# Kernel optimization log

Hardware: AMD Instinct MI355X
Metric: run time of the kernel (lower is better)

## Reference

```python
import jax, jax.numpy as jnp
import numpy as np

N_U, N_I, D = 30000, 15000, 64
L = 2                 # propagation layers (self.l)
TEMP = 0.2
LAMBDA1, LAMBDA2 = 0.2, 1e-7
H, F = 4, 16          # GAT heads x per-head dim; H*F == D
NEG_SLOPE = 0.2
AVG_DEG = 16
B = 2048


def setup_inputs() -> dict:
    key = jax.random.key(0)
    ks = jax.random.split(key, 10)
    rng = np.random.default_rng(0)
    E_u_0 = jax.random.normal(ks[0], (N_U, D), jnp.float32) * 0.1
    E_i_0 = jax.random.normal(ks[1], (N_I, D), jnp.float32) * 0.1
    # sparse normalized bipartite adjacency (adj_norm) as an edge list
    nnz = N_U * AVG_DEG
    u_idx = np.repeat(np.arange(N_U), AVG_DEG)
    i_idx = rng.integers(0, N_I, nnz)
    deg_u = np.bincount(u_idx, minlength=N_U)
    deg_i = np.maximum(np.bincount(i_idx, minlength=N_I), 1)
    vals = (1.0 / np.sqrt(deg_u[u_idx] * deg_i[i_idx])).astype(np.float32)
    # GAT graph on n_u+n_i nodes: bipartite edges both directions + self-loops
    n = N_U + N_I
    src = np.concatenate([u_idx, i_idx + N_U, np.arange(n)]).astype(np.int32)
    dst = np.concatenate([i_idx + N_U, u_idx, np.arange(n)]).astype(np.int32)
    # GAT parameters (fresh each forward in original, so just random)
    W = jax.random.normal(ks[2], (D, H * F), jnp.float32) / np.sqrt(D)
    attn_l = jax.random.normal(ks[3], (H, F), jnp.float32) * 0.1
    attn_r = jax.random.normal(ks[4], (H, F), jnp.float32) * 0.1
    uids = jax.random.randint(ks[5], (B,), 0, N_U, jnp.int32)
    iids = jax.random.randint(ks[6], (B,), 0, N_I, jnp.int32)
    pos = jax.random.randint(ks[7], (B,), 0, N_I, jnp.int32)
    neg = jax.random.randint(ks[8], (B,), 0, N_I, jnp.int32)
    return dict(E_u_0=E_u_0, E_i_0=E_i_0, adj_vals=jnp.asarray(vals),
                W=W, attn_l=attn_l, attn_r=attn_r,
                u_idx=jnp.asarray(u_idx, jnp.int32), i_idx=jnp.asarray(i_idx, jnp.int32),
                src=jnp.asarray(src), dst=jnp.asarray(dst),
                uids=uids, iids=iids, pos=pos, neg=neg)


def gat_layer(h, src, dst, W, attn_l, attn_r, n_nodes):
    # GATConv: project, per-edge attention, neighborhood softmax, scatter-agg
    feat = (h @ W).reshape(-1, H, F)                      # [N,H,F]
    el = (feat * attn_l).sum(-1)                          # [N,H]
    er = (feat * attn_r).sum(-1)                          # [N,H]
    e = jax.nn.leaky_relu(el[src] + er[dst], NEG_SLOPE)   # [E,H]
    e_max = jax.ops.segment_max(e, dst, num_segments=n_nodes)
    a = jnp.exp(e - e_max[dst])
    denom = jax.ops.segment_sum(a, dst, num_segments=n_nodes)
    a = a / denom[dst]                                    # self-loops => denom>0
    out = jax.ops.segment_sum(a[:, :, None] * feat[src], dst, num_segments=n_nodes)
    return jax.nn.elu(out.reshape(-1, H * F))             # [N,D]


def _forward(E_u_0, E_i_0, adj_vals, W, attn_l, attn_r,
             u_idx, i_idx, src, dst, uids, iids, pos, neg):
    n = N_U + N_I
    Eu, Ei = E_u_0, E_i_0
    sum_Eu, sum_Ei = E_u_0, E_i_0
    sum_Gu, sum_Gi = E_u_0, E_i_0
    for _ in range(L):
        # LightGCN spmm propagation: Z_u = A @ E_i, Z_i = A.T @ E_u
        Zu = jax.ops.segment_sum(adj_vals[:, None] * Ei[i_idx], u_idx, num_segments=N_U)
        Zi = jax.ops.segment_sum(adj_vals[:, None] * Eu[u_idx], i_idx, num_segments=N_I)
        ls1 = gat_layer(jnp.concatenate([Eu, Ei], 0), src, dst, W, attn_l, attn_r, n)
        Gu, Gi = ls1[:N_U], ls1[N_U:]
        Eu, Ei = Zu + Eu, Zi + Ei
        sum_Eu = sum_Eu + Eu
        sum_Ei = sum_Ei + Ei
        sum_Gu = sum_Gu + Gu
        sum_Gi = sum_Gi + Gi
    log_eps = jnp.float32(np.log(1e-8))
    # InfoNCE: log(sum(exp(s)) + 1e-8) == logaddexp(logsumexp(s), log(1e-8))
    lse_u = jax.scipy.special.logsumexp(sum_Gu[uids] @ sum_Eu.T / TEMP, axis=1)
    lse_i = jax.scipy.special.logsumexp(sum_Gi[iids] @ sum_Ei.T / TEMP, axis=1)
    neg_score = jnp.logaddexp(lse_u, log_eps).mean() + jnp.logaddexp(lse_i, log_eps).mean()
    pos_score = ((sum_Gu[uids] * sum_Eu[uids]).sum(1) / TEMP).mean() \
              + ((sum_Gi[iids] * sum_Ei[iids]).sum(1) / TEMP).mean()
    loss_s = -pos_score + neg_score
    # BPR loss
    u_emb = sum_Eu[uids]
    diff = (u_emb * sum_Ei[pos]).sum(-1) - (u_emb * sum_Ei[neg]).sum(-1)
    loss_r = -jax.nn.log_sigmoid(diff).mean()
    # L2 reg over nn.Parameters (E_u_0, E_i_0 only)
    loss_reg = LAMBDA2 * ((E_u_0 ** 2).sum() + (E_i_0 ** 2).sum())
    loss = loss_r + LAMBDA1 * loss_s + loss_reg
    return loss, loss_r, LAMBDA1 * loss_s


def reference(E_u_0, E_i_0, adj_vals, W, attn_l, attn_r,
              u_idx, i_idx, src, dst, uids, iids, pos, neg):
    return _forward(E_u_0, E_i_0, adj_vals, W, attn_l, attn_r,
                    u_idx, i_idx, src, dst, uids, iids, pos, neg)
```

## Files before the change

kernel.cpp:

```cpp
#include <hip/hip_runtime.h>
#include <math.h>

#define N_U 30000
#define N_I 15000
#define N_TOT 45000
#define D 64
#define NNZ 480000
#define B 2048
#define INV_TEMP 5.0f
#define LOG_EPS -18.420680743952367f
#define NEG_SLOPE 0.2f
#define LAMBDA1 0.2f
#define LAMBDA2 1e-7f

#define NSP 128
#define RSP_U 235
#define RSP_I 118
#define PAD_U 30016
#define PAD_I 15040
#define SCALE_LOG2 7.2134752044448170f
#define LN2F 0.6931471805599453f

typedef __attribute__((ext_vector_type(8))) short short8;
typedef __attribute__((ext_vector_type(4))) float f32x4;

__device__ inline float wred(float v) {
#pragma unroll
  for (int o = 32; o > 0; o >>= 1) v += __shfl_down(v, o, 64);
  return v;
}

__device__ inline float leaky(float v) { return (v >= 0.f) ? v : NEG_SLOPE * v; }

__device__ inline void atomMaxF(float* a, float v) {
  if (v >= 0.f) atomicMax((int*)a, __float_as_int(v));
  else atomicMin((unsigned int*)a, __float_as_uint(v));
}

__device__ inline unsigned short f2bf(float x) {
  unsigned u = __float_as_uint(x);
  unsigned r = u + 0x7FFFu + ((u >> 16) & 1u);
  return (unsigned short)(r >> 16);
}
__device__ inline float bf2f(unsigned short h) {
  return __uint_as_float(((unsigned)h) << 16);
}

__global__ void k_init(const float* __restrict__ Eu0, const float* __restrict__ Ei0,
                       float* fU, float* fI, float* sEu, float* sEi,
                       float* sGu, float* sGi, int* deg, float* acc) {
  int t = blockIdx.x * 256 + threadIdx.x;
  if (t < 16) acc[t] = (t >= 8) ? -INFINITY : 0.f;
  if (t < N_I) deg[t] = 0;
  if (t < N_U * D) {
    int n = t >> 6, c = t & 63;
    float v = Eu0[t];
    fU[(size_t)n * 128 + c] = v;
    sEu[t] = v; sGu[t] = v;
  } else if (t < N_TOT * D) {
    int j = t - N_U * D;
    int n = j >> 6, c = j & 63;
    float v = Ei0[j];
    fI[(size_t)n * 128 + c] = v;
    sEi[j] = v; sGi[j] = v;
  }
}

__global__ void k_deg(const int* __restrict__ ii, int* deg) {
  int e = blockIdx.x * 256 + threadIdx.x;
  if (e < NNZ) atomicAdd(&deg[ii[e]], 1);
}

__global__ void k_scan(const int* __restrict__ deg, int* rowptr, int* cursor) {
  __shared__ int tsum[1024];
  const int CHUNK = 15;
  int tid = threadIdx.x;
  int base = tid * CHUNK;
  int s = 0;
#pragma unroll
  for (int k = 0; k < CHUNK; k++) {
    int idx = base + k;
    s += (idx < N_I) ? deg[idx] : 0;
  }
  tsum[tid] = s;
  __syncthreads();
  for (int o = 1; o < 1024; o <<= 1) {
    int x = (tid >= o) ? tsum[tid - o] : 0;
    __syncthreads();
    tsum[tid] += x;
    __syncthreads();
  }
  int excl = tsum[tid] - s;
#pragma unroll
  for (int k = 0; k < CHUNK; k++) {
    int idx = base + k;
    if (idx < N_I) {
      rowptr[idx] = excl;
      cursor[idx] = excl;
      excl += deg[idx];
    }
  }
  if (tid == 1023) rowptr[N_I] = tsum[1023];
}

__global__ void k_fill(const int* __restrict__ ii, const float* __restrict__ vals,
                       int* cursor, int* u_srt, float* v_srt) {
  int e = blockIdx.x * 256 + threadIdx.x;
  if (e < NNZ) {
    int pos = atomicAdd(&cursor[ii[e]], 1);
    u_srt[pos] = e >> 4;
    v_srt[pos] = vals[e];
  }
}

__global__ void k_feat(float* __restrict__ fU, float* __restrict__ fI,
                       const float* __restrict__ W, const float* __restrict__ al,
                       const float* __restrict__ ar,
                       float* __restrict__ el, float* __restrict__ er) {
  __shared__ float Ws[64 * 64];
  __shared__ float hs[16][64];
  int tid = threadIdx.x;
  for (int t = tid; t < 1024; t += 256) ((float4*)Ws)[t] = ((const float4*)W)[t];
  int g = tid >> 6, c = tid & 63;
  int n0 = blockIdx.x * 16 + g * 4;
  float* rows[4];
#pragma unroll
  for (int j = 0; j < 4; j++) {
    int node = n0 + j;
    rows[j] = nullptr;
    if (node < N_TOT) {
      rows[j] = (node < N_U) ? (fU + (size_t)node * 128) : (fI + (size_t)(node - N_U) * 128);
      hs[g * 4 + j][c] = rows[j][c];
    }
  }
  __syncthreads();
  float a0 = 0.f, a1 = 0.f, a2 = 0.f, a3 = 0.f;
#pragma unroll 8
  for (int k = 0; k < 64; ++k) {
    float w = Ws[k * 64 + c];
    a0 = fmaf(hs[g * 4 + 0][k], w, a0);
    a1 = fmaf(hs[g * 4 + 1][k], w, a1);
    a2 = fmaf(hs[g * 4 + 2][k], w, a2);
    a3 = fmaf(hs[g * 4 + 3][k], w, a3);
  }
  float accs[4] = {a0, a1, a2, a3};
  float alc = al[c], arc = ar[c];
#pragma unroll
  for (int j = 0; j < 4; j++) {
    int node = n0 + j;
    if (node >= N_TOT) continue;
    rows[j][64 + c] = accs[j];
    float pl = accs[j] * alc;
    float pr = accs[j] * arc;
#pragma unroll
    for (int o = 8; o >= 1; o >>= 1) {
      pl += __shfl_down(pl, o, 16);
      pr += __shfl_down(pr, o, 16);
    }
    if ((c & 15) == 0) {
      el[node * 4 + (c >> 4)] = pl;
      er[node * 4 + (c >> 4)] = pr;
    }
  }
}

__global__ void k_elmax(const float* __restrict__ el, float* __restrict__ dst) {
  __shared__ float red[4][4];
  int tid = threadIdx.x;
  int lane = tid & 63, wv = tid >> 6;
  float mx = -INFINITY;
  for (int t = blockIdx.x * 256 + tid; t < N_TOT * 4; t += 64 * 256)
    mx = fmaxf(mx, el[t]);
#pragma unroll
  for (int o = 4; o < 64; o <<= 1) mx = fmaxf(mx, __shfl_xor(mx, o, 64));
  if (lane < 4) red[wv][lane] = mx;
  __syncthreads();
  if (tid < 4) {
    float m2 = fmaxf(fmaxf(red[0][tid], red[1][tid]), fmaxf(red[2][tid], red[3][tid]));
    atomMaxF(dst + tid, m2);
  }
}

__global__ void k_layer(const float* __restrict__ fU_cur, const float* __restrict__ fI_cur,
                        const float* __restrict__ el, const float* __restrict__ er,
                        const float* __restrict__ vals, const int* __restrict__ ii,
                        const int* __restrict__ rowptr, const int* __restrict__ u_srt,
                        const float* __restrict__ v_srt,
                        const float* __restrict__ elmx,
                        float* __restrict__ fU_nxt, float* __restrict__ fI_nxt,
                        float* __restrict__ sEu, float* __restrict__ sEi,
                        float* __restrict__ sGu, float* __restrict__ sGi,
                        unsigned short* __restrict__ EuH, unsigned short* __restrict__ EuL,
                        unsigned short* __restrict__ EiH, unsigned short* __restrict__ EiL,
                        float* __restrict__ normU, float* __restrict__ normI) {
  int t = blockIdx.x * 256 + threadIdx.x;
  int node = t >> 6, c = t & 63;
  if (node >= N_TOT) return;
  int h = c >> 4;

  if (node < N_U) {
    int u = node;
    float eru = er[u * 4 + h];
    float m = leaky(elmx[h] + eru);
    const float* selfrow = fU_cur + (size_t)u * 128;
    float aself = __expf(leaky(el[u * 4 + h] + eru) - m);

    int idx[16]; float vv[16];
#pragma unroll
    for (int k = 0; k < 16; k++) { idx[k] = ii[u * 16 + k]; vv[k] = vals[u * 16 + k]; }
    float av[16];
#pragma unroll
    for (int k = 0; k < 16; k++)
      av[k] = __expf(leaky(el[(idx[k] + N_U) * 4 + h] + eru) - m);

    float den = aself;
#pragma unroll
    for (int k = 0; k < 16; k++) den += av[k];

    float o0 = aself * selfrow[64 + c], o1 = 0.f;
    float z0 = 0.f, z1 = 0.f;
#pragma unroll
    for (int k = 0; k < 16; k += 2) {
      const float* rA = fI_cur + (size_t)idx[k] * 128;
      const float* rB = fI_cur + (size_t)idx[k + 1] * 128;
      float eA = rA[c], fA = rA[64 + c];
      float eB = rB[c], fB = rB[64 + c];
      z0 = fmaf(vv[k], eA, z0);
      z1 = fmaf(vv[k + 1], eB, z1);
      o0 = fmaf(av[k], fA, o0);
      o1 = fmaf(av[k + 1], fB, o1);
    }
    float o = (o0 + o1) / den;
    float g = (o > 0.f) ? o : expm1f(o);
    float e_new = selfrow[c] + z0 + z1;
    fU_nxt[(size_t)u * 128 + c] = e_new;
    size_t off = (size_t)u * D + c;
    float s_final = sEu[off] + e_new;
    sEu[off] = s_final;
    sGu[off] += g;
    if (EuH) {
      unsigned short hi = f2bf(s_final);
      EuH[off] = hi;
      EuL[off] = f2bf(s_final - bf2f(hi));
      float n2 = wred(s_final * s_final);
      if (c == 0) normU[u] = n2;
    }
  } else {
    int i = node - N_U;
    float eri = er[node * 4 + h];
    float m = leaky(elmx[h] + eri);
    const float* selfrow = fI_cur + (size_t)i * 128;
    float aself = __expf(leaky(el[node * 4 + h] + eri) - m);
    float den0 = aself, den1 = 0.f;
    float o0 = aself * selfrow[64 + c], o1 = 0.f;
    float z0 = 0.f, z1 = 0.f;
    int r0 = rowptr[i], r1 = rowptr[i + 1];
    int r = r0;
    for (; r + 3 < r1; r += 4) {
      int u0 = u_srt[r], u1 = u_srt[r + 1], u2 = u_srt[r + 2], u3 = u_srt[r + 3];
      float v0 = v_srt[r], v1 = v_srt[r + 1], v2 = v_srt[r + 2], v3 = v_srt[r + 3];
      float a0 = __expf(leaky(el[u0 * 4 + h] + eri) - m);
      float a1 = __expf(leaky(el[u1 * 4 + h] + eri) - m);
      float a2 = __expf(leaky(el[u2 * 4 + h] + eri) - m);
      float a3 = __expf(leaky(el[u3 * 4 + h] + eri) - m);
      const float* R0 = fU_cur + (size_t)u0 * 128;
      const float* R1 = fU_cur + (size_t)u1 * 128;
      const float* R2 = fU_cur + (size_t)u2 * 128;
      const float* R3 = fU_cur + (size_t)u3 * 128;
      float e0 = R0[c], f0 = R0[64 + c];
      float e1 = R1[c], f1 = R1[64 + c];
      float e2 = R2[c], f2 = R2[64 + c];
      float e3 = R3[c], f3 = R3[64 + c];
      z0 = fmaf(v0, e0, z0); z1 = fmaf(v1, e1, z1);
      z0 = fmaf(v2, e2, z0); z1 = fmaf(v3, e3, z1);
      den0 += a0 + a2; den1 += a1 + a3;
      o0 = fmaf(a0, f0, o0); o1 = fmaf(a1, f1, o1);
      o0 = fmaf(a2, f2, o0); o1 = fmaf(a3, f3, o1);
    }
    for (; r < r1; r++) {
      int u0 = u_srt[r];
      float v0 = v_srt[r];
      float a0 = __expf(leaky(el[u0 * 4 + h] + eri) - m);
      const float* R0 = fU_cur + (size_t)u0 * 128;
      float e0 = R0[c], f0 = R0[64 + c];
      z0 = fmaf(v0, e0, z0);
      den0 += a0;
      o0 = fmaf(a0, f0, o0);
    }
    float o = (o0 + o1) / (den0 + den1);
    float g = (o > 0.f) ? o : expm1f(o);
    float e_new = selfrow[c] + z0 + z1;
    fI_nxt[(size_t)i * 128 + c] = e_new;
    size_t off = (size_t)i * D + c;
    float s_final = sEi[off] + e_new;
    sEi[off] = s_final;
    sGi[off] += g;
    if (EiH) {
      unsigned short hi = f2bf(s_final);
      EiH[off] = hi;
      EiL[off] = f2bf(s_final - bf2f(hi));
      float n2 = wred(s_final * s_final);
      if (c == 0) normI[i] = n2;
    }
  }
}

__global__ void k_normreg(const float* __restrict__ nU, const float* __restrict__ nI,
                          const float* __restrict__ Eu0, const float* __restrict__ Ei0,
                          float* __restrict__ acc) {
  __shared__ float red[4][3];
  int tid = threadIdx.x;
  int lane = tid & 63, wv = tid >> 6;
  float mu = 0.f, mi = 0.f, s = 0.f;
  for (int t = blockIdx.x * 256 + tid; t < N_U; t += 128 * 256) mu = fmaxf(mu, nU[t]);
  for (int t = blockIdx.x * 256 + tid; t < N_I; t += 128 * 256) mi = fmaxf(mi, nI[t]);
  const float4* A = (const float4*)Eu0;
  const float4* Bp = (const float4*)Ei0;
  const int nA = N_U * 16, nTot = N_TOT * 16;
  for (int t = blockIdx.x * 256 + tid; t < nTot; t += 128 * 256) {
    float4 v = (t < nA) ? A[t] : Bp[t - nA];
    s += v.x * v.x + v.y * v.y + v.z * v.z + v.w * v.w;
  }
#pragma unroll
  for (int o = 32; o > 0; o >>= 1) {
    mu = fmaxf(mu, __shfl_down(mu, o, 64));
    mi = fmaxf(mi, __shfl_down(mi, o, 64));
    s += __shfl_down(s, o, 64);
  }
  if (lane == 0) { red[wv][0] = mu; red[wv][1] = mi; red[wv][2] = s; }
  __syncthreads();
  if (tid == 0) {
    float a = fmaxf(fmaxf(red[0][0], red[1][0]), fmaxf(red[2][0], red[3][0]));
    float b = fmaxf(fmaxf(red[0][1], red[1][1]), fmaxf(red[2][1], red[3][1]));
    float ssum = red[0][2] + red[1][2] + red[2][2] + red[3][2];
    atomMaxF(acc + 6, a);
    atomMaxF(acc + 7, b);
    unsafeAtomicAdd(acc + 5, ssum);
  }
}

__global__ void k_cvt_q(const float* __restrict__ sGu, const float* __restrict__ sGi,
                        const int* __restrict__ uids, const int* __restrict__ iids,
                        unsigned short* __restrict__ QuH, unsigned short* __restrict__ QuL,
                        unsigned short* __restrict__ QiH, unsigned short* __restrict__ QiL,
                        const float* __restrict__ acc,
                        float* __restrict__ M0u, float* __restrict__ M0i) {
  int lane = threadIdx.x & 63, wv = threadIdx.x >> 6;
  int row = blockIdx.x * 4 + wv;
  int side = row >> 11;
  int b = row & (B - 1);
  int id = side ? iids[b] : uids[b];
  float x = (side ? sGi : sGu)[(size_t)id * 64 + lane] * SCALE_LOG2;
  unsigned short hi = f2bf(x);
  unsigned short lo = f2bf(x - bf2f(hi));
  if (side) { QiH[(size_t)b * 64 + lane] = hi; QiL[(size_t)b * 64 + lane] = lo; }
  else      { QuH[(size_t)b * 64 + lane] = hi; QuL[(size_t)b * 64 + lane] = lo; }
  float n2 = wred(x * x);
  if (lane == 0) {
    float en2 = side ? acc[7] : acc[6];
    float M0 = sqrtf(n2) * sqrtf(en2) * 1.01f + 1.0f;
    (side ? M0i : M0u)[b] = M0;
  }
}

__global__ __launch_bounds__(256, 2) void k_lse_mfma(
    const unsigned short* __restrict__ QuH, const unsigned short* __restrict__ QuL,
    const unsigned short* __restrict__ EuHp, const unsigned short* __restrict__ EuLp,
    const unsigned short* __restrict__ QiH, const unsigned short* __restrict__ QiL,
    const unsigned short* __restrict__ EiHp, const unsigned short* __restrict__ EiLp,
    const float* __restrict__ M0u, const float* __restrict__ M0i,
    float* __restrict__ psU, float* __restrict__ psI) {
  int z = blockIdx.z;
  const unsigned short* Qhi = z ? QiH : QuH;
  const unsigned short* Qlo = z ? QiL : QuL;
  const unsigned short* Ehi = z ? EiHp : EuHp;
  const unsigned short* Elo = z ? EiLp : EuLp;
  const float* M0arr = z ? M0i : M0u;
  float* part_s = z ? psI : psU;
  int n_rows = z ? N_I : N_U;
  int rows_per_split = z ? RSP_I : RSP_U;

  int tid = threadIdx.x;
  int wave = tid >> 6, lane = tid & 63;
  int l15 = lane & 15, quad = lane >> 4;
  int qbase = (blockIdx.x * 4 + wave) * 128;
  int split = blockIdx.y;
  int row0 = split * rows_per_split;
  int row_end = min(row0 + rows_per_split, n_rows);
  int rows = row_end - row0; if (rows < 0) rows = 0;
  int total = (rows + 15) >> 4;
  int ntail = rows & 15;

  float ss[8][4];
#pragma unroll
  for (int t = 0; t < 8; t++)
#pragma unroll
    for (int g = 0; g < 4; g++) ss[t][g] = 0.f;

  if (total > 0) {
    short8 ah[8][2], al[8][2];
#pragma unroll
    for (int t = 0; t < 8; t++)
#pragma unroll
      for (int c = 0; c < 2; c++) {
        size_t idx = (size_t)(qbase + t * 16 + l15) * 64 + c * 32 + quad * 8;
        ah[t][c] = *(const short8*)(Qhi + idx);
        al[t][c] = *(const short8*)(Qlo + idx);
      }

    f32x4 cinit[8];
#pragma unroll
    for (int t = 0; t < 8; t++)
#pragma unroll
      for (int g = 0; g < 4; g++)
        cinit[t][g] = -M0arr[qbase + t * 16 + quad * 4 + g];

    const unsigned short* ph = Ehi + (size_t)(row0 + l15) * 64 + quad * 8;
    const unsigned short* pl = Elo + (size_t)(row0 + l15) * 64 + quad * 8;

    short8 cb0 = *(const short8*)(ph);
    short8 cb1 = *(const short8*)(ph + 32);
    short8 cb2 = *(const short8*)(pl);
    short8 cb3 = *(const short8*)(pl + 32);
    ph += 1024; pl += 1024;

    for (int it = 0; it < total - 1; it++) {
      short8 nb0 = *(const short8*)(ph);
      short8 nb1 = *(const short8*)(ph + 32);
      short8 nb2 = *(const short8*)(pl);
      short8 nb3 = *(const short8*)(pl + 32);
      ph += 1024; pl += 1024;
#pragma unroll
      for (int t = 0; t < 8; t++) {
        f32x4 acc = cinit[t];
        acc = __builtin_amdgcn_mfma_f32_16x16x32_bf16(ah[t][0], cb0, acc, 0, 0, 0);
        acc = __builtin_amdgcn_mfma_f32_16x16x32_bf16(ah[t][1], cb1, acc, 0, 0, 0);
        acc = __builtin_amdgcn_mfma_f32_16x16x32_bf16(al[t][0], cb0, acc, 0, 0, 0);
        acc = __builtin_amdgcn_mfma_f32_16x16x32_bf16(al[t][1], cb1, acc, 0, 0, 0);
        acc = __builtin_amdgcn_mfma_f32_16x16x32_bf16(ah[t][0], cb2, acc, 0, 0, 0);
        acc = __builtin_amdgcn_mfma_f32_16x16x32_bf16(ah[t][1], cb3, acc, 0, 0, 0);
#pragma unroll
        for (int g = 0; g < 4; g++)
          ss[t][g] += exp2f(acc[g]);
      }
      cb0 = nb0; cb1 = nb1; cb2 = nb2; cb3 = nb3;
    }
    {
      bool valid = (ntail == 0) || (l15 < ntail);
#pragma unroll
      for (int t = 0; t < 8; t++) {
        f32x4 acc = cinit[t];
        acc = __builtin_amdgcn_mfma_f32_16x16x32_bf16(ah[t][0], cb0, acc, 0, 0, 0);
        acc = __builtin_amdgcn_mfma_f32_16x16x32_bf16(ah[t][1], cb1, acc, 0, 0, 0);
        acc = __builtin_amdgcn_mfma_f32_16x16x32_bf16(al[t][0], cb0, acc, 0, 0, 0);
        acc = __builtin_amdgcn_mfma_f32_16x16x32_bf16(al[t][1], cb1, acc, 0, 0, 0);
        acc = __builtin_amdgcn_mfma_f32_16x16x32_bf16(ah[t][0], cb2, acc, 0, 0, 0);
        acc = __builtin_amdgcn_mfma_f32_16x16x32_bf16(ah[t][1], cb3, acc, 0, 0, 0);
#pragma unroll
        for (int g = 0; g < 4; g++) {
          float e = exp2f(acc[g]);
          ss[t][g] += valid ? e : 0.f;
        }
      }
    }
  }

#pragma unroll
  for (int off = 1; off < 16; off <<= 1) {
#pragma unroll
    for (int t = 0; t < 8; t++)
#pragma unroll
      for (int g = 0; g < 4; g++)
        ss[t][g] += __shfl_xor(ss[t][g], off, 64);
  }

  if (l15 == 0) {
#pragma unroll
    for (int t = 0; t < 8; t++)
#pragma unroll
      for (int g = 0; g < 4; g++) {
        int q = qbase + t * 16 + quad * 4 + g;
        part_s[(size_t)split * B + q] = ss[t][g];
      }
  }
}

__global__ void k_small(const float* __restrict__ sEu, const float* __restrict__ sEi,
                        const float* __restrict__ sGu, const float* __restrict__ sGi,
                        const int* __restrict__ uids, const int* __restrict__ iids,
                        const int* __restrict__ pos, const int* __restrict__ neg,
                        const float* __restrict__ psU, const float* __restrict__ psI,
                        const float* __restrict__ M0u, const float* __restrict__ M0i,
                        float* acc) {
  int b = blockIdx.x * 256 + threadIdx.x;
  float du = 0.f, di = 0.f, nu = 0.f, ni = 0.f, bpr = 0.f;
  if (b < B) {
    float su = 0.f, si = 0.f;
    for (int s2 = 0; s2 < NSP; s2++) su += psU[(size_t)s2 * B + b];
    for (int s2 = 0; s2 < NSP; s2++) si += psI[(size_t)s2 * B + b];
    float lseu = M0u[b] * LN2F + logf(su);
    float lsei = M0i[b] * LN2F + logf(si);
    nu = fmaxf(lseu, LOG_EPS) + log1pf(expf(-fabsf(lseu - LOG_EPS)));
    ni = fmaxf(lsei, LOG_EPS) + log1pf(expf(-fabsf(lsei - LOG_EPS)));

    int u = uids[b], it = iids[b], p = pos[b], ng = neg[b];
    const float4* gu = (const float4*)(sGu + (size_t)u * D);
    const float4* eu = (const float4*)(sEu + (size_t)u * D);
    const float4* gi = (const float4*)(sGi + (size_t)it * D);
    const float4* ei = (const float4*)(sEi + (size_t)it * D);
    const float4* ep = (const float4*)(sEi + (size_t)p * D);
    const float4* en = (const float4*)(sEi + (size_t)ng * D);
    float diff = 0.f;
#pragma unroll
    for (int k = 0; k < 16; k++) {
      float4 a = gu[k], b4 = eu[k];
      du += a.x * b4.x + a.y * b4.y + a.z * b4.z + a.w * b4.w;
      float4 c = gi[k], d4 = ei[k];
      di += c.x * d4.x + c.y * d4.y + c.z * d4.z + c.w * d4.w;
      float4 e = ep[k], f = en[k];
      diff += b4.x * (e.x - f.x) + b4.y * (e.y - f.y) + b4.z * (e.z - f.z) + b4.w * (e.w - f.w);
    }
    bpr = (diff > 0.f) ? log1pf(expf(-diff)) : (-diff + log1pf(expf(diff)));
  }
  du = wred(du); di = wred(di); nu = wred(nu); ni = wred(ni); bpr = wred(bpr);
  if ((threadIdx.x & 63) == 0) {
    unsafeAtomicAdd(acc + 0, du);
    unsafeAtomicAdd(acc + 1, di);
    unsafeAtomicAdd(acc + 2, nu);
    unsafeAtomicAdd(acc + 3, ni);
    unsafeAtomicAdd(acc + 4, bpr);
  }
}

__global__ void k_final(const float* __restrict__ acc, float* __restrict__ out) {
  float pos_score = (acc[0] + acc[1]) * (INV_TEMP / (float)B);
  float neg_score = (acc[2] + acc[3]) / (float)B;
  float loss_s = neg_score - pos_score;
  float loss_r = acc[4] / (float)B;
  float reg = LAMBDA2 * acc[5];
  out[0] = loss_r + LAMBDA1 * loss_s + reg;
  out[1] = loss_r;
  out[2] = LAMBDA1 * loss_s;
}

extern "C" void kernel_launch(void* const* d_in, const int* in_sizes, int n_in,
                              void* d_out, int out_size, void* d_ws, size_t ws_size,
                              hipStream_t stream) {
  const float* Eu0  = (const float*)d_in[0];
  const float* Ei0  = (const float*)d_in[1];
  const float* vals = (const float*)d_in[2];
  const float* W    = (const float*)d_in[3];
  const float* al   = (const float*)d_in[4];
  const float* ar   = (const float*)d_in[5];
  const int* ii     = (const int*)d_in[7];
  const int* uids   = (const int*)d_in[10];
  const int* iids   = (const int*)d_in[11];
  const int* pos    = (const int*)d_in[12];
  const int* neg    = (const int*)d_in[13];
  float* out = (float*)d_out;

  char* base = (char*)d_ws;
  size_t off = 0;
  auto alloc = [&](size_t bytes) -> void* {
    void* p = base + off;
    off = (off + bytes + 255) & ~(size_t)255;
    return p;
  };
  float* fU_a = (float*)alloc((size_t)N_U * 128 * 4);
  float* fU_b = (float*)alloc((size_t)N_U * 128 * 4);
  float* fI_a = (float*)alloc((size_t)N_I * 128 * 4);
  float* fI_b = (float*)alloc((size_t)N_I * 128 * 4);
  float* sEu  = (float*)alloc((size_t)N_U * D * 4);
  float* sEi  = (float*)alloc((size_t)N_I * D * 4);
  float* sGu  = (float*)alloc((size_t)N_U * D * 4);
  float* sGi  = (float*)alloc((size_t)N_I * D * 4);
  float* el   = (float*)alloc((size_t)N_TOT * 4 * 4);
  float* er   = (float*)alloc((size_t)N_TOT * 4 * 4);
  float* psU  = (float*)alloc((size_t)B * NSP * 4);
  float* psI  = (float*)alloc((size_t)B * NSP * 4);
  float* M0u  = (float*)alloc((size_t)B * 4);
  float* M0i  = (float*)alloc((size_t)B * 4);
  float* normU= (float*)alloc((size_t)N_U * 4);
  float* normI= (float*)alloc((size_t)N_I * 4);
  float* acc  = (float*)alloc(16 * 4);
  int* deg    = (int*)alloc((size_t)N_I * 4);
  int* cursor = (int*)alloc((size_t)N_I * 4);
  int* rowptr = (int*)alloc((size_t)(N_I + 1) * 4);
  int* u_srt  = (int*)alloc((size_t)NNZ * 4);
  float* v_srt= (float*)alloc((size_t)NNZ * 4);
  unsigned short* EuH = (unsigned short*)alloc((size_t)PAD_U * 64 * 2);
  unsigned short* EuL = (unsigned short*)alloc((size_t)PAD_U * 64 * 2);
  unsigned short* EiH = (unsigned short*)alloc((size_t)PAD_I * 64 * 2);
  unsigned short* EiL = (unsigned short*)alloc((size_t)PAD_I * 64 * 2);
  unsigned short* QuH = (unsigned short*)alloc((size_t)B * 64 * 2);
  unsigned short* QuL = (unsigned short*)alloc((size_t)B * 64 * 2);
  unsigned short* QiH = (unsigned short*)alloc((size_t)B * 64 * 2);
  unsigned short* QiL = (unsigned short*)alloc((size_t)B * 64 * 2);

  k_init<<<(N_TOT * D + 255) / 256, 256, 0, stream>>>(Eu0, Ei0, fU_a, fI_a, sEu, sEi, sGu, sGi,
                                                      deg, acc);
  k_deg<<<(NNZ + 255) / 256, 256, 0, stream>>>(ii, deg);
  k_scan<<<1, 1024, 0, stream>>>(deg, rowptr, cursor);
  k_fill<<<(NNZ + 255) / 256, 256, 0, stream>>>(ii, vals, cursor, u_srt, v_srt);

  float* cu = fU_a; float* ci = fI_a;
  float* nu = fU_b; float* ni = fI_b;
  for (int l = 0; l < 2; ++l) {
    float* elmx = acc + 8 + 4 * l;
    bool last = (l == 1);
    k_feat<<<(N_TOT + 15) / 16, 256, 0, stream>>>(cu, ci, W, al, ar, el, er);
    k_elmax<<<64, 256, 0, stream>>>(el, elmx);
    k_layer<<<(N_TOT * D) / 256, 256, 0, stream>>>(
        cu, ci, el, er, vals, ii, rowptr, u_srt, v_srt, elmx,
        nu, ni, sEu, sEi, sGu, sGi,
        last ? EuH : nullptr, last ? EuL : nullptr,
        last ? EiH : nullptr, last ? EiL : nullptr,
        normU, normI);
    float* t1 = cu; cu = nu; nu = t1;
    float* t2 = ci; ci = ni; ni = t2;
  }

  k_normreg<<<128, 256, 0, stream>>>(normU, normI, Eu0, Ei0, acc);
  k_cvt_q<<<(2 * B) / 4, 256, 0, stream>>>(sGu, sGi, uids, iids, QuH, QuL, QiH, QiL, acc, M0u, M0i);
  k_lse_mfma<<<dim3(B / 512, NSP, 2), 256, 0, stream>>>(QuH, QuL, EuH, EuL,
                                                        QiH, QiL, EiH, EiL,
                                                        M0u, M0i, psU, psI);
  k_small<<<B / 256, 256, 0, stream>>>(sEu, sEi, sGu, sGi, uids, iids, pos, neg,
                                       psU, psI, M0u, M0i, acc);
  k_final<<<1, 1, 0, stream>>>(acc, out);
}
```

Before: 446.0 us.

## Precompute per-edge GAT attention and gather packed bf16 neighbor features

```diff
diff --git a/kernel.cpp b/kernel.cpp
--- a/kernel.cpp
+++ b/kernel.cpp
@@ -104,16 +104,18 @@
 }
 
 __global__ void k_fill(const int* __restrict__ ii, const float* __restrict__ vals,
-                       int* cursor, int* u_srt, float* v_srt) {
+                       int* cursor, int* u_srt, float* v_srt, int* pos2) {
   int e = blockIdx.x * 256 + threadIdx.x;
   if (e < NNZ) {
     int pos = atomicAdd(&cursor[ii[e]], 1);
     u_srt[pos] = e >> 4;
     v_srt[pos] = vals[e];
+    pos2[e] = pos;
   }
 }
 
 __global__ void k_feat(float* __restrict__ fU, float* __restrict__ fI,
+                       unsigned int* __restrict__ gU, unsigned int* __restrict__ gI,
                        const float* __restrict__ W, const float* __restrict__ al,
                        const float* __restrict__ ar,
                        float* __restrict__ el, float* __restrict__ er) {
@@ -124,12 +126,19 @@
   int g = tid >> 6, c = tid & 63;
   int n0 = blockIdx.x * 16 + g * 4;
   float* rows[4];
+  unsigned int* grows[4];
 #pragma unroll
   for (int j = 0; j < 4; j++) {
     int node = n0 + j;
-    rows[j] = nullptr;
+    rows[j] = nullptr; grows[j] = nullptr;
     if (node < N_TOT) {
-      rows[j] = (node < N_U) ? (fU + (size_t)node * 128) : (fI + (size_t)(node - N_U) * 128);
+      if (node < N_U) {
+        rows[j] = fU + (size_t)node * 128;
+        grows[j] = gU + (size_t)node * 64;
+      } else {
+        rows[j] = fI + (size_t)(node - N_U) * 128;
+        grows[j] = gI + (size_t)(node - N_U) * 64;
+      }
       hs[g * 4 + j][c] = rows[j][c];
     }
   }
@@ -150,6 +159,7 @@
     int node = n0 + j;
     if (node >= N_TOT) continue;
     rows[j][64 + c] = accs[j];
+    grows[j][c] = ((unsigned)f2bf(accs[j]) << 16) | (unsigned)f2bf(hs[g * 4 + j][c]);
     float pl = accs[j] * alc;
     float pr = accs[j] * arc;
 #pragma unroll
@@ -181,11 +191,40 @@
   }
 }
 
+__global__ void k_attn(const float* __restrict__ el, const float* __restrict__ er,
+                       const float* __restrict__ elmx, const int* __restrict__ ii,
+                       const int* __restrict__ pos2,
+                       float* __restrict__ a_user, float* __restrict__ a_item) {
+  int e = blockIdx.x * 256 + threadIdx.x;
+  if (e >= NNZ) return;
+  int u = e >> 4;
+  int i = ii[e];
+  int p = pos2[e];
+  float4 elu = ((const float4*)el)[u];
+  float4 eru = ((const float4*)er)[u];
+  float4 eli = ((const float4*)el)[N_U + i];
+  float4 eri = ((const float4*)er)[N_U + i];
+  float m0 = elmx[0], m1 = elmx[1], m2 = elmx[2], m3 = elmx[3];
+  float4 au, ai;
+  au.x = __expf(leaky(eli.x + eru.x) - leaky(m0 + eru.x));
+  au.y = __expf(leaky(eli.y + eru.y) - leaky(m1 + eru.y));
+  au.z = __expf(leaky(eli.z + eru.z) - leaky(m2 + eru.z));
+  au.w = __expf(leaky(eli.w + eru.w) - leaky(m3 + eru.w));
+  ai.x = __expf(leaky(elu.x + eri.x) - leaky(m0 + eri.x));
+  ai.y = __expf(leaky(elu.y + eri.y) - leaky(m1 + eri.y));
+  ai.z = __expf(leaky(elu.z + eri.z) - leaky(m2 + eri.z));
+  ai.w = __expf(leaky(elu.w + eri.w) - leaky(m3 + eri.w));
+  ((float4*)a_user)[e] = au;
+  ((float4*)a_item)[p] = ai;
+}
+
 __global__ void k_layer(const float* __restrict__ fU_cur, const float* __restrict__ fI_cur,
+                        const unsigned int* __restrict__ gU, const unsigned int* __restrict__ gI,
                         const float* __restrict__ el, const float* __restrict__ er,
                         const float* __restrict__ vals, const int* __restrict__ ii,
                         const int* __restrict__ rowptr, const int* __restrict__ u_srt,
                         const float* __restrict__ v_srt,
+                        const float* __restrict__ a_user, const float* __restrict__ a_item,
                         const float* __restrict__ elmx,
                         float* __restrict__ fU_nxt, float* __restrict__ fI_nxt,
                         float* __restrict__ sEu, float* __restrict__ sEi,
@@ -209,22 +248,21 @@
 #pragma unroll
     for (int k = 0; k < 16; k++) { idx[k] = ii[u * 16 + k]; vv[k] = vals[u * 16 + k]; }
     float av[16];
-#pragma unroll
-    for (int k = 0; k < 16; k++)
-      av[k] = __expf(leaky(el[(idx[k] + N_U) * 4 + h] + eru) - m);
-
     float den = aself;
 #pragma unroll
-    for (int k = 0; k < 16; k++) den += av[k];
+    for (int k = 0; k < 16; k++) {
+      av[k] = a_user[(size_t)(u * 16 + k) * 4 + h];
+      den += av[k];
+    }
 
     float o0 = aself * selfrow[64 + c], o1 = 0.f;
     float z0 = 0.f, z1 = 0.f;
 #pragma unroll
     for (int k = 0; k < 16; k += 2) {
-      const float* rA = fI_cur + (size_t)idx[k] * 128;
-      const float* rB = fI_cur + (size_t)idx[k + 1] * 128;
-      float eA = rA[c], fA = rA[64 + c];
-      float eB = rB[c], fB = rB[64 + c];
+      unsigned gA = gI[(size_t)idx[k] * 64 + c];
+      unsigned gB = gI[(size_t)idx[k + 1] * 64 + c];
+      float eA = __uint_as_float(gA << 16), fA = __uint_as_float(gA & 0xFFFF0000u);
+      float eB = __uint_as_float(gB << 16), fB = __uint_as_float(gB & 0xFFFF0000u);
       z0 = fmaf(vv[k], eA, z0);
       z1 = fmaf(vv[k + 1], eB, z1);
       o0 = fmaf(av[k], fA, o0);
@@ -259,18 +297,18 @@
     for (; r + 3 < r1; r += 4) {
       int u0 = u_srt[r], u1 = u_srt[r + 1], u2 = u_srt[r + 2], u3 = u_srt[r + 3];
       float v0 = v_srt[r], v1 = v_srt[r + 1], v2 = v_srt[r + 2], v3 = v_srt[r + 3];
-      float a0 = __expf(leaky(el[u0 * 4 + h] + eri) - m);
-      float a1 = __expf(leaky(el[u1 * 4 + h] + eri) - m);
-      float a2 = __expf(leaky(el[u2 * 4 + h] + eri) - m);
-      float a3 = __expf(leaky(el[u3 * 4 + h] + eri) - m);
-      const float* R0 = fU_cur + (size_t)u0 * 128;
-      const float* R1 = fU_cur + (size_t)u1 * 128;
-      const float* R2 = fU_cur + (size_t)u2 * 128;
-      const float* R3 = fU_cur + (size_t)u3 * 128;
-      float e0 = R0[c], f0 = R0[64 + c];
-      float e1 = R1[c], f1 = R1[64 + c];
-      float e2 = R2[c], f2 = R2[64 + c];
-      float e3 = R3[c], f3 = R3[64 + c];
+      float a0 = a_item[(size_t)(r + 0) * 4 + h];
+      float a1 = a_item[(size_t)(r + 1) * 4 + h];
+      float a2 = a_item[(size_t)(r + 2) * 4 + h];
+      float a3 = a_item[(size_t)(r + 3) * 4 + h];
+      unsigned g0 = gU[(size_t)u0 * 64 + c];
+      unsigned g1 = gU[(size_t)u1 * 64 + c];
+      unsigned g2 = gU[(size_t)u2 * 64 + c];
+      unsigned g3 = gU[(size_t)u3 * 64 + c];
+      float e0 = __uint_as_float(g0 << 16), f0 = __uint_as_float(g0 & 0xFFFF0000u);
+      float e1 = __uint_as_float(g1 << 16), f1 = __uint_as_float(g1 & 0xFFFF0000u);
+      float e2 = __uint_as_float(g2 << 16), f2 = __uint_as_float(g2 & 0xFFFF0000u);
+      float e3 = __uint_as_float(g3 << 16), f3 = __uint_as_float(g3 & 0xFFFF0000u);
       z0 = fmaf(v0, e0, z0); z1 = fmaf(v1, e1, z1);
       z0 = fmaf(v2, e2, z0); z1 = fmaf(v3, e3, z1);
       den0 += a0 + a2; den1 += a1 + a3;
@@ -280,9 +318,9 @@
     for (; r < r1; r++) {
       int u0 = u_srt[r];
       float v0 = v_srt[r];
-      float a0 = __expf(leaky(el[u0 * 4 + h] + eri) - m);
-      const float* R0 = fU_cur + (size_t)u0 * 128;
-      float e0 = R0[c], f0 = R0[64 + c];
+      float a0 = a_item[(size_t)r * 4 + h];
+      unsigned g0 = gU[(size_t)u0 * 64 + c];
+      float e0 = __uint_as_float(g0 << 16), f0 = __uint_as_float(g0 & 0xFFFF0000u);
       z0 = fmaf(v0, e0, z0);
       den0 += a0;
       o0 = fmaf(a0, f0, o0);
@@ -570,6 +608,10 @@
   float* fU_b = (float*)alloc((size_t)N_U * 128 * 4);
   float* fI_a = (float*)alloc((size_t)N_I * 128 * 4);
   float* fI_b = (float*)alloc((size_t)N_I * 128 * 4);
+  unsigned int* gU = (unsigned int*)alloc((size_t)N_U * 64 * 4);
+  unsigned int* gI = (unsigned int*)alloc((size_t)N_I * 64 * 4);
+  float* a_user = (float*)alloc((size_t)NNZ * 4 * 4);
+  float* a_item = (float*)alloc((size_t)NNZ * 4 * 4);
   float* sEu  = (float*)alloc((size_t)N_U * D * 4);
   float* sEi  = (float*)alloc((size_t)N_I * D * 4);
   float* sGu  = (float*)alloc((size_t)N_U * D * 4);
@@ -588,6 +630,7 @@
   int* rowptr = (int*)alloc((size_t)(N_I + 1) * 4);
   int* u_srt  = (int*)alloc((size_t)NNZ * 4);
   float* v_srt= (float*)alloc((size_t)NNZ * 4);
+  int* pos2   = (int*)alloc((size_t)NNZ * 4);
   unsigned short* EuH = (unsigned short*)alloc((size_t)PAD_U * 64 * 2);
   unsigned short* EuL = (unsigned short*)alloc((size_t)PAD_U * 64 * 2);
   unsigned short* EiH = (unsigned short*)alloc((size_t)PAD_I * 64 * 2);
@@ -597,21 +640,22 @@
   unsigned short* QiH = (unsigned short*)alloc((size_t)B * 64 * 2);
   unsigned short* QiL = (unsigned short*)alloc((size_t)B * 64 * 2);
 
-  k_init<<<(N_TOT * D + 255) / 256, 256, 0, stream>>>(Eu0, Ei0, fU_a, fI_a, sEu, sEi, sGu, sGi,
-                                                      deg, acc);
+  k_init<<<(N_TOT * D + 255) / 256, 256, 0, stream>>>(Eu0, Ei0, fU_a, fI_a,
+                                                      sEu, sEi, sGu, sGi, deg, acc);
   k_deg<<<(NNZ + 255) / 256, 256, 0, stream>>>(ii, deg);
   k_scan<<<1, 1024, 0, stream>>>(deg, rowptr, cursor);
-  k_fill<<<(NNZ + 255) / 256, 256, 0, stream>>>(ii, vals, cursor, u_srt, v_srt);
+  k_fill<<<(NNZ + 255) / 256, 256, 0, stream>>>(ii, vals, cursor, u_srt, v_srt, pos2);
 
   float* cu = fU_a; float* ci = fI_a;
   float* nu = fU_b; float* ni = fI_b;
   for (int l = 0; l < 2; ++l) {
     float* elmx = acc + 8 + 4 * l;
     bool last = (l == 1);
-    k_feat<<<(N_TOT + 15) / 16, 256, 0, stream>>>(cu, ci, W, al, ar, el, er);
+    k_feat<<<(N_TOT + 15) / 16, 256, 0, stream>>>(cu, ci, gU, gI, W, al, ar, el, er);
     k_elmax<<<64, 256, 0, stream>>>(el, elmx);
+    k_attn<<<(NNZ + 255) / 256, 256, 0, stream>>>(el, er, elmx, ii, pos2, a_user, a_item);
     k_layer<<<(N_TOT * D) / 256, 256, 0, stream>>>(
-        cu, ci, el, er, vals, ii, rowptr, u_srt, v_srt, elmx,
+        cu, ci, gU, gI, el, er, vals, ii, rowptr, u_srt, v_srt, a_user, a_item, elmx,
         nu, ni, sEu, sEi, sGu, sGi,
         last ? EuH : nullptr, last ? EuL : nullptr,
         last ? EiH : nullptr, last ? EiL : nullptr,
```

New measurement: 424.1 us. 4.9% less time.
